# Optimization experiments

Measured on AMD Instinct MI355X. Metric: run time of the kernel, lower is better.

## Reference

```python
import jax, jax.numpy as jnp
import numpy as np

B, S, D, M = 4, 8192, 1024, 512  # batch, seq_len, dim, memory_dim (= dim // 2)
LN_EPS = 1e-5


def _layernorm(z, g, b):
    mu = jnp.mean(z, axis=-1, keepdims=True)
    var = jnp.var(z, axis=-1, keepdims=True)
    return (z - mu) * jax.lax.rsqrt(var + LN_EPS) * g + b


def setup_inputs() -> dict:
    key = jax.random.key(0)
    ks = jax.random.split(key, 16)
    s_d = 1.0 / np.sqrt(D)
    s_m = 1.0 / np.sqrt(M)
    return {
        "x": jax.random.normal(ks[0], (B, S, D), jnp.float32),
        "Wd": jax.random.normal(ks[1], (D, M), jnp.float32) * s_d,
        "bd": jnp.zeros((M,), jnp.float32),
        "Wq": jax.random.normal(ks[2], (M, M), jnp.float32) * s_m,
        "bq": jnp.zeros((M,), jnp.float32),
        "Wk": jax.random.normal(ks[3], (M, M), jnp.float32) * s_m,
        "bk": jnp.zeros((M,), jnp.float32),
        "Wv": jax.random.normal(ks[4], (M, M), jnp.float32) * s_m,
        "bv": jnp.zeros((M,), jnp.float32),
        "gq": jnp.ones((M,), jnp.float32),
        "bq_ln": jnp.zeros((M,), jnp.float32),
        "gk": jnp.ones((M,), jnp.float32),
        "bk_ln": jnp.zeros((M,), jnp.float32),
        "W1": jax.random.normal(ks[5], (M, M), jnp.float32) * s_m,  # MemoryMLP layer 1
        "W2": jax.random.normal(ks[6], (M, M), jnp.float32) * s_m,  # MemoryMLP layer 2
        "Wu": jax.random.normal(ks[7], (M, D), jnp.float32) * s_m,
        "bu": jnp.zeros((D,), jnp.float32),
        "adaptive_lr": jnp.float32(0.01),
        "forget_factor": jnp.float32(0.1),
    }


def reference(x, Wd, bd, Wq, bq, Wk, bk, Wv, bv, gq, bq_ln, gk, bk_ln,
              W1, W2, Wu, bu, adaptive_lr, forget_factor):
    # project to memory dim: [B,S,M]
    h = jnp.einsum('bsd,dm->bsm', x, Wd) + bd
    q = _layernorm(h @ Wq + bq, gq, bq_ln)
    k = _layernorm(h @ Wk + bk, gk, bk_ln)
    v = h @ Wv + bv
    # MemoryMLP prediction on keys (depth 2, gelu between)
    pred = jax.nn.gelu(k @ W1) @ W2
    # surprise (negative gradient direction of MSE store loss), lr-scaled
    u = adaptive_lr * (v - pred)                       # inputs to scan [B,S,M]
    g = jax.nn.sigmoid(forget_factor)                  # scalar retention gate
    gates = jnp.full((B, S, 1), g, dtype=x.dtype)
    # gated linear recurrence s_t = g_t * s_{t-1} + u_t  (AssocScan math)
    def combine(a, c):
        g1, u1 = a
        g2, u2 = c
        return (g1 * g2, u1 * g2 + u2)
    _, mem = jax.lax.associative_scan(combine, (gates, u), axis=1)  # [B,S,M]
    # query-gated readout, project up, residual ('mal' integration)
    retrieved = q * mem
    out = x + jnp.einsum('bsm,md->bsd', retrieved, Wu) + bu
    return out
```

## Files before the change

### kernel.cpp

```cpp
#include <hip/hip_runtime.h>
#include <hip/hip_bf16.h>
#include <cstdint>


typedef unsigned short u16;
typedef __attribute__((ext_vector_type(8))) short short8;
typedef __attribute__((ext_vector_type(4))) float f32x4;

#define R_ROWS 32768
#define S_LEN 8192
#define D_DIM 1024
#define M_DIM 512

__device__ __forceinline__ float bf2f(u16 u) {
  union { unsigned int i; float f; } v; v.i = ((unsigned int)u) << 16; return v.f;
}
__device__ __forceinline__ u16 f2bf(float f) {
  union { float f; unsigned int i; } v; v.f = f;
  unsigned int r = v.i + 0x7fff + ((v.i >> 16) & 1);
  return (u16)(r >> 16);
}

__global__ __launch_bounds__(256)
void conv_f2b(const float* __restrict__ src, u16* __restrict__ dst) {
  const long i = ((long)blockIdx.x * 256 + threadIdx.x) * 8;
  short8 o;
#pragma unroll
  for (int j = 0; j < 8; ++j) o[j] = (short)f2bf(src[i + j]);
  *(short8*)(dst + i) = o;
}

__global__ __launch_bounds__(256)
void transpose_f2b(const float* __restrict__ src, u16* __restrict__ dst,
                   int rows, int cols) {
  __shared__ u16 tile[32][33];
  const int tx = threadIdx.x & 31;
  const int ty = threadIdx.x >> 5;
  const int bx = blockIdx.x, by = blockIdx.y;
  const int c = bx * 32 + tx;
#pragma unroll
  for (int i = 0; i < 32; i += 8)
    tile[ty + i][tx] = f2bf(src[(long)(by * 32 + ty + i) * cols + c]);
  __syncthreads();
  const int c2 = by * 32 + tx;
#pragma unroll
  for (int i = 0; i < 32; i += 8)
    dst[(long)(bx * 32 + ty + i) * rows + c2] = tile[tx][ty + i];
}

__global__ __launch_bounds__(256)
void concat3(const float* __restrict__ a, const float* __restrict__ b,
             const float* __restrict__ c, float* __restrict__ o) {
  const int i = blockIdx.x * 256 + threadIdx.x;
  o[i] = (i < 512) ? a[i] : (i < 1024) ? b[i - 512] : c[i - 1024];
}

template <int EPI>
__global__ __launch_bounds__(256, 2)
void gemm_bt(const u16* __restrict__ A, const u16* __restrict__ BT,
             const float* __restrict__ bias, void* __restrict__ Cv,
             const int K, const int N,
             const void* __restrict__ auxv, const float* __restrict__ sclr) {
  __shared__ short As[128 * 32];
  __shared__ short Bs[128 * 32];
  const int tid = threadIdx.x;
  const int lane = tid & 63;
  const int wid = tid >> 6;
  const int l15 = lane & 15;
  const int lg = lane >> 4;
  const int wr = wid >> 1;
  const int wc = wid & 1;
  const long am0 = (long)blockIdx.x * 128;
  const long bn0 = (long)blockIdx.y * 128;
  const int srow = tid >> 2;
  const int scol = (tid & 3) * 8;

  f32x4 acc[4][4];
#pragma unroll
  for (int i = 0; i < 4; ++i)
#pragma unroll
    for (int j = 0; j < 4; ++j) acc[i][j] = (f32x4){0.f, 0.f, 0.f, 0.f};

  for (int k0 = 0; k0 < K; k0 += 32) {
#pragma unroll
    for (int p = 0; p < 2; ++p) {
      const u16* ga = A + (am0 + p * 64 + srow) * K + (k0 + scol);
      const u16* gb = BT + (bn0 + p * 64 + srow) * K + (k0 + scol);
      char* la = ((char*)As) + p * 4096 + wid * 1024;
      char* lb = ((char*)Bs) + p * 4096 + wid * 1024;
      __builtin_amdgcn_global_load_lds(
          (const __attribute__((address_space(1))) void*)ga,
          (__attribute__((address_space(3))) void*)la, 16, 0, 0);
      __builtin_amdgcn_global_load_lds(
          (const __attribute__((address_space(1))) void*)gb,
          (__attribute__((address_space(3))) void*)lb, 16, 0, 0);
    }
    __syncthreads();
    short8 af[4], bf[4];
#pragma unroll
    for (int mi = 0; mi < 4; ++mi)
      af[mi] = *(const short8*)(As + (wr * 64 + mi * 16 + l15) * 32 + lg * 8);
#pragma unroll
    for (int ni = 0; ni < 4; ++ni)
      bf[ni] = *(const short8*)(Bs + (wc * 64 + ni * 16 + l15) * 32 + lg * 8);
#pragma unroll
    for (int mi = 0; mi < 4; ++mi)
#pragma unroll
      for (int ni = 0; ni < 4; ++ni)
        acc[mi][ni] = __builtin_amdgcn_mfma_f32_16x16x32_bf16(
            af[mi], bf[ni], acc[mi][ni], 0, 0, 0);
    __syncthreads();
  }

  if constexpr (EPI == 3) {
    __shared__ float Cs[64 * 132];
    const float* xf = (const float*)auxv;
    float* Of = (float*)Cv;
    const int tcol = (tid & 31) * 4;
    const int trow = tid >> 5;
#pragma unroll
    for (int p = 0; p < 2; ++p) {
      if (wr == p) {
#pragma unroll
        for (int mi = 0; mi < 4; ++mi)
#pragma unroll
          for (int ni = 0; ni < 4; ++ni)
#pragma unroll
            for (int r = 0; r < 4; ++r)
              Cs[(mi * 16 + lg * 4 + r) * 132 + wc * 64 + ni * 16 + l15] =
                  acc[mi][ni][r];
      }
      __syncthreads();
#pragma unroll
      for (int rb = 0; rb < 64; rb += 8) {
        const int lrow = rb + trow;
        const long row = am0 + p * 64 + lrow;
        const long col = bn0 + tcol;
        f32x4 cv = *(const f32x4*)&Cs[lrow * 132 + tcol];
        const f32x4 xv = *(const f32x4*)&xf[row * N + col];
        const f32x4 bv = *(const f32x4*)&bias[col];
#pragma unroll
        for (int j = 0; j < 4; ++j) cv[j] += xv[j] + bv[j];
        *(f32x4*)&Of[row * N + col] = cv;
      }
      __syncthreads();
    }
    return;
  }

  float lr = 0.f;
  if (EPI == 2) lr = *sclr;
#pragma unroll
  for (int mi = 0; mi < 4; ++mi) {
    const long row0 = am0 + wr * 64 + mi * 16 + lg * 4;
#pragma unroll
    for (int ni = 0; ni < 4; ++ni) {
      const long col = bn0 + wc * 64 + ni * 16 + l15;
      const float bb = bias ? bias[col] : 0.f;
#pragma unroll
      for (int r = 0; r < 4; ++r) {
        const long row = row0 + r;
        float c = acc[mi][ni][r] + bb;
        if (EPI == 1) {
          c = 0.5f * c * (1.f + tanhf(0.7978845608028654f * (c + 0.044715f * c * c * c)));
        } else if (EPI == 2) {
          c = lr * (bf2f(((const u16*)auxv)[row * N + col]) - c);
        }
        if (EPI == 4) {
          const long sel = col >> 9;
          ((u16*)Cv)[sel * ((long)R_ROWS * M_DIM) + row * M_DIM + (col & 511)] =
              f2bf(c);
        } else {
          ((u16*)Cv)[row * N + col] = f2bf(c);
        }
      }
    }
  }
}

__global__ __launch_bounds__(256)
void ln_qk(u16* __restrict__ q, u16* __restrict__ k,
           const float* __restrict__ gq, const float* __restrict__ bq,
           const float* __restrict__ gk, const float* __restrict__ bk) {
  const int wid = threadIdx.x >> 6, lane = threadIdx.x & 63;
  long job = (long)blockIdx.x * 4 + wid;
  u16* base;
  const float *g, *b;
  if (job < R_ROWS) { base = q; g = gq; b = bq; }
  else { base = k; g = gk; b = bk; job -= R_ROWS; }
  u16* p = base + job * M_DIM + lane * 8;
  short8 zv = *(short8*)p;
  float z[8], s = 0.f, s2 = 0.f;
#pragma unroll
  for (int i = 0; i < 8; ++i) {
    z[i] = bf2f((u16)zv[i]);
    s += z[i];
    s2 += z[i] * z[i];
  }
#pragma unroll
  for (int off = 32; off >= 1; off >>= 1) {
    s += __shfl_xor(s, off);
    s2 += __shfl_xor(s2, off);
  }
  const float mu = s * (1.f / 512.f);
  const float inv = rsqrtf(s2 * (1.f / 512.f) - mu * mu + 1e-5f);
#pragma unroll
  for (int i = 0; i < 8; ++i) {
    float y = (z[i] - mu) * inv * g[lane * 8 + i] + b[lane * 8 + i];
    zv[i] = (short)f2bf(y);
  }
  *(short8*)p = zv;
}

#define SCAN_CH 32
#define SCAN_L (S_LEN / SCAN_CH)
#define SCAN_W 128

__global__ __launch_bounds__(512)
void scan_mul(const u16* __restrict__ u, const u16* __restrict__ q,
              u16* __restrict__ retr, const float* __restrict__ ffp) {
  const int m = threadIdx.x;
  const int b = blockIdx.x / SCAN_CH;
  const int ch = blockIdx.x % SCAN_CH;
  const float g = 1.f / (1.f + __expf(-*ffp));
  const long base = ((long)b * S_LEN) * M_DIM + m;
  const int t0 = ch * SCAN_L;
  const int tw = (t0 >= SCAN_W) ? (t0 - SCAN_W) : 0;
  float s = 0.f;
#pragma unroll 8
  for (int t = tw; t < t0; ++t) s = g * s + bf2f(u[base + (long)t * M_DIM]);
#pragma unroll 8
  for (int t = t0; t < t0 + SCAN_L; ++t) {
    const long idx = base + (long)t * M_DIM;
    s = g * s + bf2f(u[idx]);
    retr[idx] = f2bf(bf2f(q[idx]) * s);
  }
}

extern "C" void kernel_launch(void* const* d_in, const int* in_sizes, int n_in,
                              void* d_out, int out_size, void* d_ws,
                              size_t ws_size, hipStream_t stream) {
  const float* x = (const float*)d_in[0];
  const float* Wd = (const float*)d_in[1];
  const float* bd = (const float*)d_in[2];
  const float* Wq = (const float*)d_in[3];
  const float* bq = (const float*)d_in[4];
  const float* Wk = (const float*)d_in[5];
  const float* bk = (const float*)d_in[6];
  const float* Wv = (const float*)d_in[7];
  const float* bv = (const float*)d_in[8];
  const float* gq = (const float*)d_in[9];
  const float* bq_ln = (const float*)d_in[10];
  const float* gk = (const float*)d_in[11];
  const float* bk_ln = (const float*)d_in[12];
  const float* W1 = (const float*)d_in[13];
  const float* W2 = (const float*)d_in[14];
  const float* Wu = (const float*)d_in[15];
  const float* bu = (const float*)d_in[16];
  const float* lr = (const float*)d_in[17];
  const float* ff = (const float*)d_in[18];

  char* w = (char*)d_ws;
  auto alloc = [&](size_t bytes) {
    char* p = w;
    w += (bytes + 255) & ~(size_t)255;
    return (u16*)p;
  };
  u16* WdT = alloc(512 * 1024 * 2);
  u16* WqkvT = alloc((size_t)1536 * 512 * 2);
  u16* W1T = alloc(512 * 512 * 2);
  u16* W2T = alloc(512 * 512 * 2);
  u16* WuT = alloc(1024 * 512 * 2);
  float* bqkv = (float*)alloc(1536 * 4);
  const size_t act = (size_t)R_ROWS * M_DIM * 2;
  u16* hB = alloc(act);
  u16* qB = alloc(act);
  u16* kB = alloc(act);
  u16* vB = alloc(act);
  u16* xb = (u16*)d_out;
  u16* t1 = hB;
  u16* uB = kB;
  u16* retr = vB;

  dim3 tb(256);
  conv_f2b<<<dim3(16384), tb, 0, stream>>>(x, xb);
  transpose_f2b<<<dim3(16, 32), tb, 0, stream>>>(Wd, WdT, 1024, 512);
  transpose_f2b<<<dim3(16, 16), tb, 0, stream>>>(Wq, WqkvT, 512, 512);
  transpose_f2b<<<dim3(16, 16), tb, 0, stream>>>(Wk, WqkvT + 512 * 512, 512, 512);
  transpose_f2b<<<dim3(16, 16), tb, 0, stream>>>(Wv, WqkvT + 2 * 512 * 512, 512, 512);
  transpose_f2b<<<dim3(16, 16), tb, 0, stream>>>(W1, W1T, 512, 512);
  transpose_f2b<<<dim3(16, 16), tb, 0, stream>>>(W2, W2T, 512, 512);
  transpose_f2b<<<dim3(32, 16), tb, 0, stream>>>(Wu, WuT, 512, 1024);
  concat3<<<dim3(6), tb, 0, stream>>>(bq, bk, bv, bqkv);

  gemm_bt<0><<<dim3(256, 4), 256, 0, stream>>>(xb, WdT, bd, hB, 1024, 512, nullptr, nullptr);
  gemm_bt<4><<<dim3(256, 12), 256, 0, stream>>>(hB, WqkvT, bqkv, qB, 512, 512, nullptr, nullptr);
  ln_qk<<<dim3(16384), 256, 0, stream>>>(qB, kB, gq, bq_ln, gk, bk_ln);
  gemm_bt<1><<<dim3(256, 4), 256, 0, stream>>>(kB, W1T, nullptr, t1, 512, 512, nullptr, nullptr);
  gemm_bt<2><<<dim3(256, 4), 256, 0, stream>>>(t1, W2T, nullptr, uB, 512, 512, vB, lr);
  scan_mul<<<dim3(4 * SCAN_CH), 512, 0, stream>>>(uB, qB, retr, ff);
  gemm_bt<3><<<dim3(256, 8), 256, 0, stream>>>(retr, WuT, bu, d_out, 512, 1024, x, nullptr);
}
```

Baseline: 372.3 us.

## Fuse x fp32-to-bf16 conversion into first GEMM and vectorize scan

Drops the separate pass that converts x to bf16. The first projection GEMM now loads fp32 x directly, packs it to bf16 in registers and writes it into shared memory, which removes a full read and write of the large input. The scan now handles two channels per thread with 32-bit loads and stores, and the residual epilogue is restaged in 32-row chunks with wider per-thread stores. The A-operand path in the first GEMM loses the asynchronous global-to-LDS copy and becomes a synchronous register path, which may stall the main loop.

Measured after the change: 388.2 us. 1.04x slower.

```diff
diff --git a/kernel.cpp b/kernel.cpp
--- a/kernel.cpp
+++ b/kernel.cpp
@@ -4,8 +4,10 @@
 
 
 typedef unsigned short u16;
+typedef unsigned int u32;
 typedef __attribute__((ext_vector_type(8))) short short8;
 typedef __attribute__((ext_vector_type(4))) float f32x4;
+typedef __attribute__((ext_vector_type(4))) u32 u32x4;
 
 #define R_ROWS 32768
 #define S_LEN 8192
@@ -20,14 +22,9 @@
   unsigned int r = v.i + 0x7fff + ((v.i >> 16) & 1);
   return (u16)(r >> 16);
 }
-
-__global__ __launch_bounds__(256)
-void conv_f2b(const float* __restrict__ src, u16* __restrict__ dst) {
-  const long i = ((long)blockIdx.x * 256 + threadIdx.x) * 8;
-  short8 o;
-#pragma unroll
-  for (int j = 0; j < 8; ++j) o[j] = (short)f2bf(src[i + j]);
-  *(short8*)(dst + i) = o;
+__device__ __forceinline__ u32 pk2(float a, float b) {
+  __hip_bfloat162 h = __float22bfloat162_rn(float2{a, b});
+  union { __hip_bfloat162 h2; u32 u; } c; c.h2 = h; return c.u;
 }
 
 __global__ __launch_bounds__(256)
@@ -55,14 +52,14 @@
   o[i] = (i < 512) ? a[i] : (i < 1024) ? b[i - 512] : c[i - 1024];
 }
 
-template <int EPI>
+template <int EPI, bool AF32>
 __global__ __launch_bounds__(256, 2)
-void gemm_bt(const u16* __restrict__ A, const u16* __restrict__ BT,
+void gemm_bt(const void* __restrict__ Av, const u16* __restrict__ BT,
              const float* __restrict__ bias, void* __restrict__ Cv,
              const int K, const int N,
              const void* __restrict__ auxv, const float* __restrict__ sclr) {
-  __shared__ short As[128 * 32];
-  __shared__ short Bs[128 * 32];
+  __shared__ __align__(16) short As[128 * 32];
+  __shared__ __align__(16) short Bs[128 * 32];
   const int tid = threadIdx.x;
   const int lane = tid & 63;
   const int wid = tid >> 6;
@@ -82,15 +79,38 @@
     for (int j = 0; j < 4; ++j) acc[i][j] = (f32x4){0.f, 0.f, 0.f, 0.f};
 
   for (int k0 = 0; k0 < K; k0 += 32) {
+    if constexpr (AF32) {
+      const float* Af = (const float*)Av;
+      const int arow = tid >> 1;
+      const int acol = (tid & 1) << 4;
+      const float* ga = Af + (am0 + arow) * K + (k0 + acol);
+      const f32x4 w0 = *(const f32x4*)ga;
+      const f32x4 w1 = *(const f32x4*)(ga + 4);
+      const f32x4 w2 = *(const f32x4*)(ga + 8);
+      const f32x4 w3 = *(const f32x4*)(ga + 12);
+      u32x4 lo, hi;
+      lo[0] = pk2(w0[0], w0[1]); lo[1] = pk2(w0[2], w0[3]);
+      lo[2] = pk2(w1[0], w1[1]); lo[3] = pk2(w1[2], w1[3]);
+      hi[0] = pk2(w2[0], w2[1]); hi[1] = pk2(w2[2], w2[3]);
+      hi[2] = pk2(w3[0], w3[1]); hi[3] = pk2(w3[2], w3[3]);
+      u32* dst = (u32*)(As + arow * 32 + acol);
+      *(u32x4*)dst = lo;
+      *(u32x4*)(dst + 4) = hi;
+    } else {
+      const u16* Ab = (const u16*)Av;
+#pragma unroll
+      for (int p = 0; p < 2; ++p) {
+        const u16* ga = Ab + (am0 + p * 64 + srow) * K + (k0 + scol);
+        char* la = ((char*)As) + p * 4096 + wid * 1024;
+        __builtin_amdgcn_global_load_lds(
+            (const __attribute__((address_space(1))) void*)ga,
+            (__attribute__((address_space(3))) void*)la, 16, 0, 0);
+      }
+    }
 #pragma unroll
     for (int p = 0; p < 2; ++p) {
-      const u16* ga = A + (am0 + p * 64 + srow) * K + (k0 + scol);
       const u16* gb = BT + (bn0 + p * 64 + srow) * K + (k0 + scol);
-      char* la = ((char*)As) + p * 4096 + wid * 1024;
       char* lb = ((char*)Bs) + p * 4096 + wid * 1024;
-      __builtin_amdgcn_global_load_lds(
-          (const __attribute__((address_space(1))) void*)ga,
-          (__attribute__((address_space(3))) void*)la, 16, 0, 0);
       __builtin_amdgcn_global_load_lds(
           (const __attribute__((address_space(1))) void*)gb,
           (__attribute__((address_space(3))) void*)lb, 16, 0, 0);
@@ -113,37 +133,40 @@
   }
 
   if constexpr (EPI == 3) {
-    __shared__ float Cs[64 * 132];
+    __shared__ float Cs[32 * 132];
     const float* xf = (const float*)auxv;
     float* Of = (float*)Cv;
-    const int tcol = (tid & 31) * 4;
-    const int trow = tid >> 5;
-#pragma unroll
-    for (int p = 0; p < 2; ++p) {
-      if (wr == p) {
-#pragma unroll
-        for (int mi = 0; mi < 4; ++mi)
+    const int orow = tid >> 3;
+    const int ocol = (tid & 7) * 16;
+#pragma unroll
+    for (int p = 0; p < 4; ++p) {
+      __syncthreads();
+      if (wr == (p >> 1)) {
+        const int mbase = (p & 1) * 2;
+#pragma unroll
+        for (int mm = 0; mm < 2; ++mm)
 #pragma unroll
           for (int ni = 0; ni < 4; ++ni)
 #pragma unroll
             for (int r = 0; r < 4; ++r)
-              Cs[(mi * 16 + lg * 4 + r) * 132 + wc * 64 + ni * 16 + l15] =
-                  acc[mi][ni][r];
+              Cs[(mm * 16 + lg * 4 + r) * 132 + wc * 64 + ni * 16 + l15] =
+                  acc[mbase + mm][ni][r];
       }
       __syncthreads();
-#pragma unroll
-      for (int rb = 0; rb < 64; rb += 8) {
-        const int lrow = rb + trow;
-        const long row = am0 + p * 64 + lrow;
-        const long col = bn0 + tcol;
-        f32x4 cv = *(const f32x4*)&Cs[lrow * 132 + tcol];
-        const f32x4 xv = *(const f32x4*)&xf[row * N + col];
-        const f32x4 bv = *(const f32x4*)&bias[col];
-#pragma unroll
-        for (int j = 0; j < 4; ++j) cv[j] += xv[j] + bv[j];
-        *(f32x4*)&Of[row * N + col] = cv;
+      const long row = am0 + p * 32 + orow;
+      const long col = bn0 + ocol;
+      const float* xr = xf + row * N + col;
+      float* op = Of + row * N + col;
+      const float* br = bias + col;
+#pragma unroll
+      for (int j = 0; j < 4; ++j) {
+        f32x4 cv = *(const f32x4*)&Cs[orow * 132 + ocol + j * 4];
+        const f32x4 xv = *(const f32x4*)(xr + j * 4);
+        const f32x4 bv = *(const f32x4*)(br + j * 4);
+#pragma unroll
+        for (int e = 0; e < 4; ++e) cv[e] += xv[e] + bv[e];
+        *(f32x4*)(op + j * 4) = cv;
       }
-      __syncthreads();
     }
     return;
   }
@@ -216,24 +239,33 @@
 #define SCAN_L (S_LEN / SCAN_CH)
 #define SCAN_W 128
 
-__global__ __launch_bounds__(512)
+__global__ __launch_bounds__(256)
 void scan_mul(const u16* __restrict__ u, const u16* __restrict__ q,
               u16* __restrict__ retr, const float* __restrict__ ffp) {
-  const int m = threadIdx.x;
+  const int m2 = threadIdx.x;
   const int b = blockIdx.x / SCAN_CH;
   const int ch = blockIdx.x % SCAN_CH;
   const float g = 1.f / (1.f + __expf(-*ffp));
-  const long base = ((long)b * S_LEN) * M_DIM + m;
+  const long base = ((long)b * S_LEN) * M_DIM + 2 * m2;
   const int t0 = ch * SCAN_L;
   const int tw = (t0 >= SCAN_W) ? (t0 - SCAN_W) : 0;
-  float s = 0.f;
+  float s0 = 0.f, s1 = 0.f;
 #pragma unroll 8
-  for (int t = tw; t < t0; ++t) s = g * s + bf2f(u[base + (long)t * M_DIM]);
+  for (int t = tw; t < t0; ++t) {
+    const u32 w = *(const u32*)(u + base + (long)t * M_DIM);
+    s0 = g * s0 + bf2f((u16)(w & 0xffff));
+    s1 = g * s1 + bf2f((u16)(w >> 16));
+  }
 #pragma unroll 8
   for (int t = t0; t < t0 + SCAN_L; ++t) {
     const long idx = base + (long)t * M_DIM;
-    s = g * s + bf2f(u[idx]);
-    retr[idx] = f2bf(bf2f(q[idx]) * s);
+    const u32 w = *(const u32*)(u + idx);
+    s0 = g * s0 + bf2f((u16)(w & 0xffff));
+    s1 = g * s1 + bf2f((u16)(w >> 16));
+    const u32 qw = *(const u32*)(q + idx);
+    const u32 o = (u32)f2bf(bf2f((u16)(qw & 0xffff)) * s0) |
+                  ((u32)f2bf(bf2f((u16)(qw >> 16)) * s1) << 16);
+    *(u32*)(retr + idx) = o;
   }
 }
 
@@ -277,13 +309,11 @@
   u16* qB = alloc(act);
   u16* kB = alloc(act);
   u16* vB = alloc(act);
-  u16* xb = (u16*)d_out;
   u16* t1 = hB;
   u16* uB = kB;
   u16* retr = vB;
 
   dim3 tb(256);
-  conv_f2b<<<dim3(16384), tb, 0, stream>>>(x, xb);
   transpose_f2b<<<dim3(16, 32), tb, 0, stream>>>(Wd, WdT, 1024, 512);
   transpose_f2b<<<dim3(16, 16), tb, 0, stream>>>(Wq, WqkvT, 512, 512);
   transpose_f2b<<<dim3(16, 16), tb, 0, stream>>>(Wk, WqkvT + 512 * 512, 512, 512);
@@ -293,11 +323,11 @@
   transpose_f2b<<<dim3(32, 16), tb, 0, stream>>>(Wu, WuT, 512, 1024);
   concat3<<<dim3(6), tb, 0, stream>>>(bq, bk, bv, bqkv);
 
-  gemm_bt<0><<<dim3(256, 4), 256, 0, stream>>>(xb, WdT, bd, hB, 1024, 512, nullptr, nullptr);
-  gemm_bt<4><<<dim3(256, 12), 256, 0, stream>>>(hB, WqkvT, bqkv, qB, 512, 512, nullptr, nullptr);
+  gemm_bt<0, true><<<dim3(256, 4), 256, 0, stream>>>(x, WdT, bd, hB, 1024, 512, nullptr, nullptr);
+  gemm_bt<4, false><<<dim3(256, 12), 256, 0, stream>>>(hB, WqkvT, bqkv, qB, 512, 512, nullptr, nullptr);
   ln_qk<<<dim3(16384), 256, 0, stream>>>(qB, kB, gq, bq_ln, gk, bk_ln);
-  gemm_bt<1><<<dim3(256, 4), 256, 0, stream>>>(kB, W1T, nullptr, t1, 512, 512, nullptr, nullptr);
-  gemm_bt<2><<<dim3(256, 4), 256, 0, stream>>>(t1, W2T, nullptr, uB, 512, 512, vB, lr);
-  scan_mul<<<dim3(4 * SCAN_CH), 512, 0, stream>>>(uB, qB, retr, ff);
-  gemm_bt<3><<<dim3(256, 8), 256, 0, stream>>>(retr, WuT, bu, d_out, 512, 1024, x, nullptr);
-}
+  gemm_bt<1, false><<<dim3(256, 4), 256, 0, stream>>>(kB, W1T, nullptr, t1, 512, 512, nullptr, nullptr);
+  gemm_bt<2, false><<<dim3(256, 4), 256, 0, stream>>>(t1, W2T, nullptr, uB, 512, 512, vB, lr);
+  scan_mul<<<dim3(4 * SCAN_CH), 256, 0, stream>>>(uB, qB, retr, ff);
+  gemm_bt<3, false><<<dim3(256, 8), 256, 0, stream>>>(retr, WuT, bu, d_out, 512, 1024, x, nullptr);
+}
```

## Read bf16 residual in output GEMM, vectorize scan to two channels per thread

Applied to the files above, without the earlier changes.

The final GEMM epilogue now reads the residual x from a bf16 copy kept in workspace instead of the fp32 input, which halves residual read traffic. The bf16 copy of x moves out of d_out into the workspace. The epilogue staging buffer shrinks to 32 rows and is processed in four passes, cutting LDS use. The scan kernel handles two adjacent channels per thread with 32-bit loads and stores, using half as many threads per block. The trade-off is that the residual is now added at bf16 precision rather than fp32, and the scan runs with fewer threads to hide its serial latency.

Result: faster. 360.0 us (-3.3%).

```diff
diff --git a/kernel.cpp b/kernel.cpp
--- a/kernel.cpp
+++ b/kernel.cpp
@@ -4,6 +4,7 @@
 
 
 typedef unsigned short u16;
+typedef unsigned int u32;
 typedef __attribute__((ext_vector_type(8))) short short8;
 typedef __attribute__((ext_vector_type(4))) float f32x4;
 
@@ -61,8 +62,8 @@
              const float* __restrict__ bias, void* __restrict__ Cv,
              const int K, const int N,
              const void* __restrict__ auxv, const float* __restrict__ sclr) {
-  __shared__ short As[128 * 32];
-  __shared__ short Bs[128 * 32];
+  __shared__ __align__(16) short As[128 * 32];
+  __shared__ __align__(16) short Bs[128 * 32];
   const int tid = threadIdx.x;
   const int lane = tid & 63;
   const int wid = tid >> 6;
@@ -113,37 +114,41 @@
   }
 
   if constexpr (EPI == 3) {
-    __shared__ float Cs[64 * 132];
-    const float* xf = (const float*)auxv;
+    __shared__ float Cs[32 * 132];
+    const u16* xb = (const u16*)auxv;
     float* Of = (float*)Cv;
+    const int trow = tid >> 5;
     const int tcol = (tid & 31) * 4;
-    const int trow = tid >> 5;
-#pragma unroll
-    for (int p = 0; p < 2; ++p) {
-      if (wr == p) {
-#pragma unroll
-        for (int mi = 0; mi < 4; ++mi)
+#pragma unroll
+    for (int p = 0; p < 4; ++p) {
+      __syncthreads();
+      if (wr == (p >> 1)) {
+        const int mbase = (p & 1) * 2;
+#pragma unroll
+        for (int mm = 0; mm < 2; ++mm)
 #pragma unroll
           for (int ni = 0; ni < 4; ++ni)
 #pragma unroll
             for (int r = 0; r < 4; ++r)
-              Cs[(mi * 16 + lg * 4 + r) * 132 + wc * 64 + ni * 16 + l15] =
-                  acc[mi][ni][r];
+              Cs[(mm * 16 + lg * 4 + r) * 132 + wc * 64 + ni * 16 + l15] =
+                  acc[mbase + mm][ni][r];
       }
       __syncthreads();
 #pragma unroll
-      for (int rb = 0; rb < 64; rb += 8) {
+      for (int rb = 0; rb < 32; rb += 8) {
         const int lrow = rb + trow;
-        const long row = am0 + p * 64 + lrow;
+        const long row = am0 + p * 32 + lrow;
         const long col = bn0 + tcol;
         f32x4 cv = *(const f32x4*)&Cs[lrow * 132 + tcol];
-        const f32x4 xv = *(const f32x4*)&xf[row * N + col];
+        const u32* xp = (const u32*)(xb + row * N + col);
+        const u32 x0 = xp[0], x1 = xp[1];
         const f32x4 bv = *(const f32x4*)&bias[col];
-#pragma unroll
-        for (int j = 0; j < 4; ++j) cv[j] += xv[j] + bv[j];
+        cv[0] += bf2f((u16)(x0 & 0xffff)) + bv[0];
+        cv[1] += bf2f((u16)(x0 >> 16)) + bv[1];
+        cv[2] += bf2f((u16)(x1 & 0xffff)) + bv[2];
+        cv[3] += bf2f((u16)(x1 >> 16)) + bv[3];
         *(f32x4*)&Of[row * N + col] = cv;
       }
-      __syncthreads();
     }
     return;
   }
@@ -216,24 +221,33 @@
 #define SCAN_L (S_LEN / SCAN_CH)
 #define SCAN_W 128
 
-__global__ __launch_bounds__(512)
+__global__ __launch_bounds__(256)
 void scan_mul(const u16* __restrict__ u, const u16* __restrict__ q,
               u16* __restrict__ retr, const float* __restrict__ ffp) {
-  const int m = threadIdx.x;
+  const int m2 = threadIdx.x;
   const int b = blockIdx.x / SCAN_CH;
   const int ch = blockIdx.x % SCAN_CH;
   const float g = 1.f / (1.f + __expf(-*ffp));
-  const long base = ((long)b * S_LEN) * M_DIM + m;
+  const long base = ((long)b * S_LEN) * M_DIM + 2 * m2;
   const int t0 = ch * SCAN_L;
   const int tw = (t0 >= SCAN_W) ? (t0 - SCAN_W) : 0;
-  float s = 0.f;
+  float s0 = 0.f, s1 = 0.f;
 #pragma unroll 8
-  for (int t = tw; t < t0; ++t) s = g * s + bf2f(u[base + (long)t * M_DIM]);
+  for (int t = tw; t < t0; ++t) {
+    const u32 w = *(const u32*)(u + base + (long)t * M_DIM);
+    s0 = g * s0 + bf2f((u16)(w & 0xffff));
+    s1 = g * s1 + bf2f((u16)(w >> 16));
+  }
 #pragma unroll 8
   for (int t = t0; t < t0 + SCAN_L; ++t) {
     const long idx = base + (long)t * M_DIM;
-    s = g * s + bf2f(u[idx]);
-    retr[idx] = f2bf(bf2f(q[idx]) * s);
+    const u32 w = *(const u32*)(u + idx);
+    s0 = g * s0 + bf2f((u16)(w & 0xffff));
+    s1 = g * s1 + bf2f((u16)(w >> 16));
+    const u32 qw = *(const u32*)(q + idx);
+    const u32 o = (u32)f2bf(bf2f((u16)(qw & 0xffff)) * s0) |
+                  ((u32)f2bf(bf2f((u16)(qw >> 16)) * s1) << 16);
+    *(u32*)(retr + idx) = o;
   }
 }
 
@@ -273,11 +287,11 @@
   u16* WuT = alloc(1024 * 512 * 2);
   float* bqkv = (float*)alloc(1536 * 4);
   const size_t act = (size_t)R_ROWS * M_DIM * 2;
+  u16* xb = alloc(2 * act);
   u16* hB = alloc(act);
   u16* qB = alloc(act);
   u16* kB = alloc(act);
   u16* vB = alloc(act);
-  u16* xb = (u16*)d_out;
   u16* t1 = hB;
   u16* uB = kB;
   u16* retr = vB;
@@ -298,6 +312,6 @@
   ln_qk<<<dim3(16384), 256, 0, stream>>>(qB, kB, gq, bq_ln, gk, bk_ln);
   gemm_bt<1><<<dim3(256, 4), 256, 0, stream>>>(kB, W1T, nullptr, t1, 512, 512, nullptr, nullptr);
   gemm_bt<2><<<dim3(256, 4), 256, 0, stream>>>(t1, W2T, nullptr, uB, 512, 512, vB, lr);
-  scan_mul<<<dim3(4 * SCAN_CH), 512, 0, stream>>>(uB, qB, retr, ff);
-  gemm_bt<3><<<dim3(256, 8), 256, 0, stream>>>(retr, WuT, bu, d_out, 512, 1024, x, nullptr);
-}
+  scan_mul<<<dim3(4 * SCAN_CH), 256, 0, stream>>>(uB, qB, retr, ff);
+  gemm_bt<3><<<dim3(256, 8), 256, 0, stream>>>(retr, WuT, bu, d_out, 512, 1024, xb, nullptr);
+}
```
